# Performance work log

Hardware: AMD Instinct MI355X
Metric: run time of the kernel (lower is better)

## Reference

```python
import jax, jax.numpy as jnp
import numpy as np

NEG_SLOPE = 0.2
EPS = 1e-12


def setup_inputs() -> dict:
    key = jax.random.key(0)
    k1, k2, k3, k4, k5 = jax.random.split(key, 5)
    N, E, IN, OUT = 100000, 1600000, 256, 64
    x = jax.random.normal(k1, (N, IN), dtype=jnp.float32)
    edge_index = jax.random.randint(k2, (2, E), 0, N, dtype=jnp.int64)
    # GATConv (heads=1) parameters: lin weight, att_src, att_dst, bias
    W = jax.random.normal(k3, (IN, OUT), dtype=jnp.float32) * (1.0 / np.sqrt(IN))
    att_src = jax.random.normal(k4, (OUT,), dtype=jnp.float32) * (1.0 / np.sqrt(OUT))
    att_dst = jax.random.normal(k5, (OUT,), dtype=jnp.float32) * (1.0 / np.sqrt(OUT))
    bias = jnp.zeros((OUT,), dtype=jnp.float32)
    return {"x": x, "edge_index": edge_index, "W": W,
            "att_src": att_src, "att_dst": att_dst, "bias": bias}


def reference(x, edge_index, W, att_src, att_dst, bias):
    N = x.shape[0]
    # PyG GATConv default add_self_loops=True
    loops = jnp.arange(N, dtype=edge_index.dtype)
    src = jnp.concatenate([edge_index[0], loops])  # source j of edge (j -> i)
    dst = jnp.concatenate([edge_index[1], loops])  # target i (softmax segment)

    h = x @ W                                      # [N, out]
    a_src = h @ att_src                            # [N] per-node source score
    a_dst = h @ att_dst                            # [N] per-node target score

    e = jax.nn.leaky_relu(a_src[src] + a_dst[dst], NEG_SLOPE)  # [E+N]
    # segment softmax over incoming edges of each destination node
    e_max = jax.ops.segment_max(e, dst, num_segments=N)
    e = jnp.exp(e - e_max[dst])
    denom = jax.ops.segment_sum(e, dst, num_segments=N)
    alpha = e / denom[dst]                         # [E+N]

    # scatter-aggregate: out[i] = sum_j alpha_ij * h[j]
    out = jax.ops.segment_sum(alpha[:, None] * h[src], dst, num_segments=N)
    out = out + bias

    # dropout (p=0.3) in eval mode is identity; then F.normalize (row-wise L2)
    nrm = jnp.sqrt(jnp.sum(out * out, axis=-1, keepdims=True))
    return out / jnp.maximum(nrm, EPS)
```

## Files before the change

### kernel.cpp

```cpp
#include <hip/hip_runtime.h>
#include <hip/hip_bf16.h>
#include <math.h>

#define NEG_SLOPE 0.2f
#define EPS_NRM 1e-12f
#define K_IN 256
#define C_OUT 64
#define KSTEP 32
#define TILE_M 128
#define LDSROW 40

typedef __attribute__((ext_vector_type(8))) short bf16x8;
typedef __attribute__((ext_vector_type(4))) float f32x4;

__device__ __forceinline__ unsigned short bf16_rne(float v) {
    unsigned u = __float_as_uint(v);
    return (unsigned short)((u + 0x7fffu + ((u >> 16) & 1u)) >> 16);
}

__global__ __launch_bounds__(256) void wsplit(
    const float* __restrict__ W, unsigned short* __restrict__ Wt_hi,
    unsigned short* __restrict__ Wt_lo)
{
    int tid = blockIdx.x * blockDim.x + threadIdx.x;
    if (tid >= K_IN * C_OUT) return;
    int k = tid >> 6, c = tid & 63;
    float v = W[tid];
    unsigned short hb = bf16_rne(v);
    float vh = __uint_as_float((unsigned)hb << 16);
    unsigned short lb = bf16_rne(v - vh);
    Wt_hi[c * K_IN + k] = hb;
    Wt_lo[c * K_IN + k] = lb;
}

__global__ __launch_bounds__(256) void gemm_att(
    const float* __restrict__ x,
    const unsigned short* __restrict__ Wt_hi,
    const unsigned short* __restrict__ Wt_lo,
    const float* __restrict__ att_s, const float* __restrict__ att_d,
    __hip_bfloat16* __restrict__ h, float* __restrict__ a_src_arr,
    float* __restrict__ a_dst_arr, int N,
    const int* __restrict__ dstA, int* __restrict__ cnt, int E)
{
    __shared__ short A_hi[TILE_M][LDSROW];
    __shared__ short A_lo[TILE_M][LDSROW];
    __shared__ short B_hi[C_OUT][LDSROW];
    __shared__ short B_lo[C_OUT][LDSROW];

    int t   = threadIdx.x;
    int w   = t >> 6;
    int l   = t & 63;
    int lm  = l & 15;
    int grp = l >> 4;
    int row0 = blockIdx.x * TILE_M;

    int xrow  = t >> 1;
    int khalf = (t & 1) * 16;
    int srow = row0 + xrow; if (srow >= N) srow = N - 1;
    const float* xp = x + (size_t)srow * K_IN + khalf;

    int wcol   = t >> 2;
    int wchunk = (t & 3) * 8;
    const unsigned short* wph = Wt_hi + wcol * K_IN + wchunk;
    const unsigned short* wpl = Wt_lo + wcol * K_IN + wchunk;

    f32x4 acc[2][4];
#pragma unroll
    for (int m = 0; m < 2; ++m)
#pragma unroll
        for (int n = 0; n < 4; ++n) acc[m][n] = (f32x4){0.f, 0.f, 0.f, 0.f};

    float4 xf0, xf1, xf2, xf3;
    bf16x8 wvh, wvl;

    auto stage = [&]() {
        short sh[16], sl[16];
        const float* fv0 = (const float*)&xf0;
        const float* fv1 = (const float*)&xf1;
        const float* fv2 = (const float*)&xf2;
        const float* fv3 = (const float*)&xf3;
#pragma unroll
        for (int i = 0; i < 4; ++i) {
            float v0 = fv0[i], v1 = fv1[i], v2 = fv2[i], v3 = fv3[i];
            unsigned short h0 = bf16_rne(v0), h1 = bf16_rne(v1),
                           h2 = bf16_rne(v2), h3 = bf16_rne(v3);
            sh[i]      = (short)h0; sh[i + 4]  = (short)h1;
            sh[i + 8]  = (short)h2; sh[i + 12] = (short)h3;
            sl[i]      = (short)bf16_rne(v0 - __uint_as_float((unsigned)h0 << 16));
            sl[i + 4]  = (short)bf16_rne(v1 - __uint_as_float((unsigned)h1 << 16));
            sl[i + 8]  = (short)bf16_rne(v2 - __uint_as_float((unsigned)h2 << 16));
            sl[i + 12] = (short)bf16_rne(v3 - __uint_as_float((unsigned)h3 << 16));
        }
        *(bf16x8*)&A_hi[xrow][khalf]     = *(bf16x8*)&sh[0];
        *(bf16x8*)&A_hi[xrow][khalf + 8] = *(bf16x8*)&sh[8];
        *(bf16x8*)&A_lo[xrow][khalf]     = *(bf16x8*)&sl[0];
        *(bf16x8*)&A_lo[xrow][khalf + 8] = *(bf16x8*)&sl[8];
        *(bf16x8*)&B_hi[wcol][wchunk] = wvh;
        *(bf16x8*)&B_lo[wcol][wchunk] = wvl;
    };

    xf0 = *(const float4*)(xp + 0);
    xf1 = *(const float4*)(xp + 4);
    xf2 = *(const float4*)(xp + 8);
    xf3 = *(const float4*)(xp + 12);
    wvh = *(const bf16x8*)(wph);
    wvl = *(const bf16x8*)(wpl);
    stage();
    __syncthreads();

    for (int k0 = 0; k0 < K_IN; k0 += KSTEP) {
        const bool more = (k0 + KSTEP) < K_IN;
        if (more) {
            xf0 = *(const float4*)(xp + k0 + KSTEP + 0);
            xf1 = *(const float4*)(xp + k0 + KSTEP + 4);
            xf2 = *(const float4*)(xp + k0 + KSTEP + 8);
            xf3 = *(const float4*)(xp + k0 + KSTEP + 12);
            wvh = *(const bf16x8*)(wph + k0 + KSTEP);
            wvl = *(const bf16x8*)(wpl + k0 + KSTEP);
        }

        int xr0 = w * 32 + lm;
        bf16x8 xh0 = *(const bf16x8*)&A_hi[xr0][grp * 8];
        bf16x8 xl0 = *(const bf16x8*)&A_lo[xr0][grp * 8];
        bf16x8 xh1 = *(const bf16x8*)&A_hi[xr0 + 16][grp * 8];
        bf16x8 xl1 = *(const bf16x8*)&A_lo[xr0 + 16][grp * 8];
#pragma unroll
        for (int n = 0; n < 4; ++n) {
            bf16x8 wh = *(const bf16x8*)&B_hi[n * 16 + lm][grp * 8];
            bf16x8 wl = *(const bf16x8*)&B_lo[n * 16 + lm][grp * 8];
            acc[0][n] = __builtin_amdgcn_mfma_f32_16x16x32_bf16(wh, xh0, acc[0][n], 0, 0, 0);
            acc[1][n] = __builtin_amdgcn_mfma_f32_16x16x32_bf16(wh, xh1, acc[1][n], 0, 0, 0);
            acc[0][n] = __builtin_amdgcn_mfma_f32_16x16x32_bf16(wl, xh0, acc[0][n], 0, 0, 0);
            acc[1][n] = __builtin_amdgcn_mfma_f32_16x16x32_bf16(wl, xh1, acc[1][n], 0, 0, 0);
            acc[0][n] = __builtin_amdgcn_mfma_f32_16x16x32_bf16(wh, xl0, acc[0][n], 0, 0, 0);
            acc[1][n] = __builtin_amdgcn_mfma_f32_16x16x32_bf16(wh, xl1, acc[1][n], 0, 0, 0);
        }

        if (more) {
            __syncthreads();
            stage();
            __syncthreads();
        }
    }

    float4 as4[4], ad4[4];
#pragma unroll
    for (int n = 0; n < 4; ++n) {
        as4[n] = *(const float4*)(att_s + n * 16 + grp * 4);
        ad4[n] = *(const float4*)(att_d + n * 16 + grp * 4);
    }
#pragma unroll
    for (int m = 0; m < 2; ++m) {
        int row = row0 + w * 32 + m * 16 + lm;
        float ps = 0.f, pd = 0.f;
#pragma unroll
        for (int n = 0; n < 4; ++n) {
            f32x4 a = acc[m][n];
            ps += a.x * as4[n].x + a.y * as4[n].y + a.z * as4[n].z + a.w * as4[n].w;
            pd += a.x * ad4[n].x + a.y * ad4[n].y + a.z * ad4[n].z + a.w * ad4[n].w;
        }
        ps += __shfl_xor(ps, 16, 64); ps += __shfl_xor(ps, 32, 64);
        pd += __shfl_xor(pd, 16, 64); pd += __shfl_xor(pd, 32, 64);
        if (row < N) {
            if (grp == 0) { a_src_arr[row] = ps; a_dst_arr[row] = pd; }
#pragma unroll
            for (int n = 0; n < 4; ++n) {
                f32x4 a = acc[m][n];
                __hip_bfloat16 b0 = __float2bfloat16(a.x);
                __hip_bfloat16 b1 = __float2bfloat16(a.y);
                __hip_bfloat16 b2 = __float2bfloat16(a.z);
                __hip_bfloat16 b3 = __float2bfloat16(a.w);
                unsigned long long pk =
                    (unsigned long long)*(unsigned short*)&b0 |
                    ((unsigned long long)*(unsigned short*)&b1 << 16) |
                    ((unsigned long long)*(unsigned short*)&b2 << 32) |
                    ((unsigned long long)*(unsigned short*)&b3 << 48);
                *(unsigned long long*)(h + (size_t)row * C_OUT + n * 16 + grp * 4) = pk;
            }
        }
    }

    int stride = gridDim.x * blockDim.x;
    for (int i = blockIdx.x * blockDim.x + t; i < E; i += stride)
        atomicAdd(&cnt[dstA[i]], 1);
}

__global__ __launch_bounds__(256) void scan_p1(
    const int* __restrict__ cnt, int* __restrict__ partials, int n)
{
    int b = blockIdx.x, t = threadIdx.x;
    int base = b * 1024;
    int s = 0;
#pragma unroll
    for (int j = 0; j < 4; ++j) {
        int i = base + t * 4 + j;
        if (i < n) s += cnt[i];
    }
    for (int d = 1; d < 64; d <<= 1) s += __shfl_xor(s, d, 64);
    __shared__ int wsum[4];
    int lane = t & 63, wid = t >> 6;
    if (lane == 0) wsum[wid] = s;
    __syncthreads();
    if (t == 0) partials[b] = wsum[0] + wsum[1] + wsum[2] + wsum[3];
}

__global__ __launch_bounds__(256) void scan_p2(int* partials, int nb)
{
    __shared__ int buf[256];
    int t = threadIdx.x;
    int v = (t < nb) ? partials[t] : 0;
    buf[t] = v;
    __syncthreads();
    for (int d = 1; d < 256; d <<= 1) {
        int w = (t >= d) ? buf[t - d] : 0;
        __syncthreads();
        buf[t] += w;
        __syncthreads();
    }
    if (t < nb) partials[t] = buf[t] - v;
}

__global__ __launch_bounds__(256) void scan_p3(
    const int* __restrict__ cnt, const int* __restrict__ partials,
    int* __restrict__ offsets, int n)
{
    int b = blockIdx.x, t = threadIdx.x;
    int base = b * 1024;
    int v[4];
    int s = 0;
#pragma unroll
    for (int j = 0; j < 4; ++j) {
        int i = base + t * 4 + j;
        v[j] = (i < n) ? cnt[i] : 0;
        s += v[j];
    }
    int lane = t & 63, wid = t >> 6;
    int incl = s;
    for (int d = 1; d < 64; d <<= 1) {
        int w = __shfl_up(incl, d, 64);
        if (lane >= d) incl += w;
    }
    __shared__ int wsum[4];
    __shared__ int wbase[4];
    if (lane == 63) wsum[wid] = incl;
    __syncthreads();
    if (t == 0) {
        int r = 0;
        for (int i = 0; i < 4; ++i) { wbase[i] = r; r += wsum[i]; }
    }
    __syncthreads();
    int run = partials[b] + wbase[wid] + (incl - s);
#pragma unroll
    for (int j = 0; j < 4; ++j) {
        int i = base + t * 4 + j;
        if (i < n) {
            offsets[i] = run;
            run += v[j];
            if (i == n - 1) offsets[n] = run;
        }
    }
}

__global__ __launch_bounds__(256) void scatter_edges(
    const int* __restrict__ srcA, const int* __restrict__ dstA,
    const int* __restrict__ offsets, int* __restrict__ cursor,
    const float* __restrict__ a_src, const float* __restrict__ a_dst,
    unsigned long long* __restrict__ csr, int E)
{
    int i = blockIdx.x * blockDim.x + threadIdx.x;
    if (i >= E) return;
    int s = srcA[i], d = dstA[i];
    float e = a_src[s] + a_dst[d];
    e = fmaxf(e, NEG_SLOPE * e);
    float w = __expf(e);
    int pos = offsets[d] + atomicAdd(&cursor[d], 1);
    unsigned long long packed =
        (unsigned long long)(unsigned)s |
        ((unsigned long long)__float_as_uint(w) << 32);
    __builtin_nontemporal_store(packed, &csr[pos]);
}

__global__ __launch_bounds__(256) void gat_pull(
    const int* __restrict__ offsets, const int2* __restrict__ csr,
    const unsigned short* __restrict__ h, const float* __restrict__ a_src,
    const float* __restrict__ a_dst, const float* __restrict__ bias,
    float* __restrict__ out, int N)
{
    int gw   = (blockIdx.x * blockDim.x + threadIdx.x) >> 6;
    int lane = threadIdx.x & 63;
    int grp  = lane >> 4;
    int gl   = lane & 15;
    int node = gw * 4 + grp;
    bool valid = node < N;
    int nv = valid ? node : 0;

    int beg = offsets[nv];
    int n   = valid ? (offsets[nv + 1] - beg) : 0;
    const int2* ce = csr + (n ? beg : 0);

    float asv = a_src[nv], adv = a_dst[nv];
    float es = asv + adv; es = fmaxf(es, NEG_SLOPE * es);
    float ws = __expf(es);
    unsigned long long hu = *(const unsigned long long*)
        (h + (size_t)nv * C_OUT + 4 * gl);
    unsigned hl = (unsigned)hu, hh = (unsigned)(hu >> 32);
    float acc0 = ws * __uint_as_float(hl << 16);
    float acc1 = ws * __uint_as_float(hl & 0xffff0000u);
    float acc2 = ws * __uint_as_float(hh << 16);
    float acc3 = ws * __uint_as_float(hh & 0xffff0000u);
    float den = ws;

    int2 c0 = ce[0];
    int2 c1 = ce[(n > 1) ? 1 : 0];
    unsigned long long u0 = *(const unsigned long long*)
        (h + (size_t)c0.x * C_OUT + 4 * gl);
    unsigned long long u1 = *(const unsigned long long*)
        (h + (size_t)c1.x * C_OUT + 4 * gl);

    for (int p = 0; p < n; p += 2) {
        int2 m0 = ce[(p + 2 < n) ? p + 2 : 0];
        int2 m1 = ce[(p + 3 < n) ? p + 3 : 0];
        unsigned long long v0 = *(const unsigned long long*)
            (h + (size_t)m0.x * C_OUT + 4 * gl);
        unsigned long long v1 = *(const unsigned long long*)
            (h + (size_t)m1.x * C_OUT + 4 * gl);

        float w0 = __int_as_float(c0.y);
        float w1 = (p + 1 < n) ? __int_as_float(c1.y) : 0.f;
        unsigned l0 = (unsigned)u0, h0 = (unsigned)(u0 >> 32);
        unsigned l1 = (unsigned)u1, h1 = (unsigned)(u1 >> 32);
        den  += w0 + w1;
        acc0 += w0 * __uint_as_float(l0 << 16)
              + w1 * __uint_as_float(l1 << 16);
        acc1 += w0 * __uint_as_float(l0 & 0xffff0000u)
              + w1 * __uint_as_float(l1 & 0xffff0000u);
        acc2 += w0 * __uint_as_float(h0 << 16)
              + w1 * __uint_as_float(h1 << 16);
        acc3 += w0 * __uint_as_float(h0 & 0xffff0000u)
              + w1 * __uint_as_float(h1 & 0xffff0000u);

        c0 = m0; c1 = m1; u0 = v0; u1 = v1;
    }

    float4 bl = *(const float4*)(bias + 4 * gl);
    float rd = 1.f / den;
    float o0 = acc0 * rd + bl.x;
    float o1 = acc1 * rd + bl.y;
    float o2 = acc2 * rd + bl.z;
    float o3 = acc3 * rd + bl.w;

    float sq = o0 * o0 + o1 * o1 + o2 * o2 + o3 * o3;
#pragma unroll
    for (int d = 1; d < 16; d <<= 1) sq += __shfl_xor(sq, d, 64);
    float rn = 1.f / fmaxf(sqrtf(sq), EPS_NRM);

    if (valid)
        *(float4*)(out + (size_t)node * C_OUT + 4 * gl) =
            make_float4(o0 * rn, o1 * rn, o2 * rn, o3 * rn);
}

extern "C" void kernel_launch(void* const* d_in, const int* in_sizes, int n_in,
                              void* d_out, int out_size, void* d_ws, size_t ws_size,
                              hipStream_t stream)
{
    const float* x     = (const float*)d_in[0];
    const int*   ei    = (const int*)d_in[1];
    const float* W     = (const float*)d_in[2];
    const float* att_s = (const float*)d_in[3];
    const float* att_d = (const float*)d_in[4];
    const float* bias  = (const float*)d_in[5];
    float*       out   = (float*)d_out;

    const int OUT = in_sizes[3];
    const int IN  = in_sizes[2] / OUT;
    const int N   = in_sizes[0] / IN;
    const int E   = in_sizes[1] / 2;

    char* w = (char*)d_ws;
    auto alloc = [&](size_t bytes) -> void* {
        void* p = (void*)w;
        w += (bytes + 255) & ~(size_t)255;
        return p;
    };
    __hip_bfloat16* h = (__hip_bfloat16*)alloc((size_t)N * C_OUT * 2);
    float* a_src  = (float*)alloc((size_t)N * 4);
    float* a_dst  = (float*)alloc((size_t)N * 4);
    int*   cnt    = (int*)alloc((size_t)N * 2 * 4);
    int*   offs   = (int*)alloc((size_t)(N + 1) * 4);
    int*   parts  = (int*)alloc(1024 * 4);
    unsigned short* Wt_hi = (unsigned short*)alloc((size_t)K_IN * C_OUT * 2);
    unsigned short* Wt_lo = (unsigned short*)alloc((size_t)K_IN * C_OUT * 2);
    unsigned long long* csr = (unsigned long long*)alloc((size_t)E * 8);
    int*   cursor = cnt + N;

    hipMemsetAsync(cnt, 0, (size_t)N * 2 * 4, stream);

    wsplit<<<(K_IN * C_OUT + 255) / 256, 256, 0, stream>>>(W, Wt_hi, Wt_lo);

    gemm_att<<<(N + TILE_M - 1) / TILE_M, 256, 0, stream>>>(
        x, Wt_hi, Wt_lo, att_s, att_d, h, a_src, a_dst, N, ei + E, cnt, E);

    int NB = (N + 1023) / 1024;
    scan_p1<<<NB, 256, 0, stream>>>(cnt, parts, N);
    scan_p2<<<1, 256, 0, stream>>>(parts, NB);
    scan_p3<<<NB, 256, 0, stream>>>(cnt, parts, offs, N);

    scatter_edges<<<(E + 255) / 256, 256, 0, stream>>>(
        ei, ei + E, offs, cursor, a_src, a_dst, csr, E);

    gat_pull<<<(N + 15) / 16, 256, 0, stream>>>(offs, (const int2*)csr,
        (const unsigned short*)h, a_src, a_dst, bias, out, N);
}
```

Baseline: 375.7 us.

## Drop LDS staging in GEMM; each wave computes 16 rows directly from registers

The x@W GEMM no longer stages tiles in shared memory with block-wide barriers. Each wave now owns 16 rows, loads its x fragments straight into MFMA operand registers, and reads the bf16 hi/lo weight fragments directly from global memory, which should hit in cache. This removes the LDS traffic and __syncthreads, and the smaller 64-row blocks mean more of them. In exchange, weight reuse across rows within a block is lost and global/L2 reads of W increase.

```diff
diff --git a/kernel.cpp b/kernel.cpp
--- a/kernel.cpp
+++ b/kernel.cpp
@@ -6,9 +6,6 @@
 #define EPS_NRM 1e-12f
 #define K_IN 256
 #define C_OUT 64
-#define KSTEP 32
-#define TILE_M 128
-#define LDSROW 40
 
 typedef __attribute__((ext_vector_type(8))) short bf16x8;
 typedef __attribute__((ext_vector_type(4))) float f32x4;
@@ -42,141 +39,85 @@
     float* __restrict__ a_dst_arr, int N,
     const int* __restrict__ dstA, int* __restrict__ cnt, int E)
 {
-    __shared__ short A_hi[TILE_M][LDSROW];
-    __shared__ short A_lo[TILE_M][LDSROW];
-    __shared__ short B_hi[C_OUT][LDSROW];
-    __shared__ short B_lo[C_OUT][LDSROW];
-
     int t   = threadIdx.x;
-    int w   = t >> 6;
+    int gw  = (blockIdx.x * blockDim.x + t) >> 6;
     int l   = t & 63;
     int lm  = l & 15;
     int grp = l >> 4;
-    int row0 = blockIdx.x * TILE_M;
-
-    int xrow  = t >> 1;
-    int khalf = (t & 1) * 16;
-    int srow = row0 + xrow; if (srow >= N) srow = N - 1;
-    const float* xp = x + (size_t)srow * K_IN + khalf;
-
-    int wcol   = t >> 2;
-    int wchunk = (t & 3) * 8;
-    const unsigned short* wph = Wt_hi + wcol * K_IN + wchunk;
-    const unsigned short* wpl = Wt_lo + wcol * K_IN + wchunk;
-
-    f32x4 acc[2][4];
-#pragma unroll
-    for (int m = 0; m < 2; ++m)
-#pragma unroll
-        for (int n = 0; n < 4; ++n) acc[m][n] = (f32x4){0.f, 0.f, 0.f, 0.f};
-
-    float4 xf0, xf1, xf2, xf3;
-    bf16x8 wvh, wvl;
-
-    auto stage = [&]() {
-        short sh[16], sl[16];
-        const float* fv0 = (const float*)&xf0;
-        const float* fv1 = (const float*)&xf1;
-        const float* fv2 = (const float*)&xf2;
-        const float* fv3 = (const float*)&xf3;
+    int row0 = gw * 16;
+
+    int srow = row0 + lm; if (srow >= N) srow = N - 1;
+    const float* xq = x + (size_t)srow * K_IN + grp * 8;
+
+    const unsigned short* wbh = Wt_hi + (size_t)lm * K_IN + grp * 8;
+    const unsigned short* wbl = Wt_lo + (size_t)lm * K_IN + grp * 8;
+
+    f32x4 acc[4];
+#pragma unroll
+    for (int n = 0; n < 4; ++n) acc[n] = (f32x4){0.f, 0.f, 0.f, 0.f};
+
+    float4 xa = *(const float4*)(xq);
+    float4 xb = *(const float4*)(xq + 4);
+
+    for (int kt = 0; kt < K_IN / 32; ++kt) {
+        float4 xa2, xb2;
+        if (kt < K_IN / 32 - 1) {
+            xa2 = *(const float4*)(xq + (kt + 1) * 32);
+            xb2 = *(const float4*)(xq + (kt + 1) * 32 + 4);
+        }
+        short sh[8], sl[8];
+        const float* fa = (const float*)&xa;
+        const float* fb = (const float*)&xb;
 #pragma unroll
         for (int i = 0; i < 4; ++i) {
-            float v0 = fv0[i], v1 = fv1[i], v2 = fv2[i], v3 = fv3[i];
-            unsigned short h0 = bf16_rne(v0), h1 = bf16_rne(v1),
-                           h2 = bf16_rne(v2), h3 = bf16_rne(v3);
-            sh[i]      = (short)h0; sh[i + 4]  = (short)h1;
-            sh[i + 8]  = (short)h2; sh[i + 12] = (short)h3;
-            sl[i]      = (short)bf16_rne(v0 - __uint_as_float((unsigned)h0 << 16));
-            sl[i + 4]  = (short)bf16_rne(v1 - __uint_as_float((unsigned)h1 << 16));
-            sl[i + 8]  = (short)bf16_rne(v2 - __uint_as_float((unsigned)h2 << 16));
-            sl[i + 12] = (short)bf16_rne(v3 - __uint_as_float((unsigned)h3 << 16));
-        }
-        *(bf16x8*)&A_hi[xrow][khalf]     = *(bf16x8*)&sh[0];
-        *(bf16x8*)&A_hi[xrow][khalf + 8] = *(bf16x8*)&sh[8];
-        *(bf16x8*)&A_lo[xrow][khalf]     = *(bf16x8*)&sl[0];
-        *(bf16x8*)&A_lo[xrow][khalf + 8] = *(bf16x8*)&sl[8];
-        *(bf16x8*)&B_hi[wcol][wchunk] = wvh;
-        *(bf16x8*)&B_lo[wcol][wchunk] = wvl;
-    };
-
-    xf0 = *(const float4*)(xp + 0);
-    xf1 = *(const float4*)(xp + 4);
-    xf2 = *(const float4*)(xp + 8);
-    xf3 = *(const float4*)(xp + 12);
-    wvh = *(const bf16x8*)(wph);
-    wvl = *(const bf16x8*)(wpl);
-    stage();
-    __syncthreads();
-
-    for (int k0 = 0; k0 < K_IN; k0 += KSTEP) {
-        const bool more = (k0 + KSTEP) < K_IN;
-        if (more) {
-            xf0 = *(const float4*)(xp + k0 + KSTEP + 0);
-            xf1 = *(const float4*)(xp + k0 + KSTEP + 4);
-            xf2 = *(const float4*)(xp + k0 + KSTEP + 8);
-            xf3 = *(const float4*)(xp + k0 + KSTEP + 12);
-            wvh = *(const bf16x8*)(wph + k0 + KSTEP);
-            wvl = *(const bf16x8*)(wpl + k0 + KSTEP);
-        }
-
-        int xr0 = w * 32 + lm;
-        bf16x8 xh0 = *(const bf16x8*)&A_hi[xr0][grp * 8];
-        bf16x8 xl0 = *(const bf16x8*)&A_lo[xr0][grp * 8];
-        bf16x8 xh1 = *(const bf16x8*)&A_hi[xr0 + 16][grp * 8];
-        bf16x8 xl1 = *(const bf16x8*)&A_lo[xr0 + 16][grp * 8];
+            float v0 = fa[i], v1 = fb[i];
+            unsigned short h0 = bf16_rne(v0), h1 = bf16_rne(v1);
+            sh[i] = (short)h0; sh[i + 4] = (short)h1;
+            sl[i]     = (short)bf16_rne(v0 - __uint_as_float((unsigned)h0 << 16));
+            sl[i + 4] = (short)bf16_rne(v1 - __uint_as_float((unsigned)h1 << 16));
+        }
+        bf16x8 xh = *(bf16x8*)&sh[0];
+        bf16x8 xl = *(bf16x8*)&sl[0];
+
+        int ko = kt * 32;
 #pragma unroll
         for (int n = 0; n < 4; ++n) {
-            bf16x8 wh = *(const bf16x8*)&B_hi[n * 16 + lm][grp * 8];
-            bf16x8 wl = *(const bf16x8*)&B_lo[n * 16 + lm][grp * 8];
-            acc[0][n] = __builtin_amdgcn_mfma_f32_16x16x32_bf16(wh, xh0, acc[0][n], 0, 0, 0);
-            acc[1][n] = __builtin_amdgcn_mfma_f32_16x16x32_bf16(wh, xh1, acc[1][n], 0, 0, 0);
-            acc[0][n] = __builtin_amdgcn_mfma_f32_16x16x32_bf16(wl, xh0, acc[0][n], 0, 0, 0);
-            acc[1][n] = __builtin_amdgcn_mfma_f32_16x16x32_bf16(wl, xh1, acc[1][n], 0, 0, 0);
-            acc[0][n] = __builtin_amdgcn_mfma_f32_16x16x32_bf16(wh, xl0, acc[0][n], 0, 0, 0);
-            acc[1][n] = __builtin_amdgcn_mfma_f32_16x16x32_bf16(wh, xl1, acc[1][n], 0, 0, 0);
-        }
-
-        if (more) {
-            __syncthreads();
-            stage();
-            __syncthreads();
-        }
-    }
-
-    float4 as4[4], ad4[4];
+            bf16x8 wh = *(const bf16x8*)(wbh + (size_t)n * 16 * K_IN + ko);
+            bf16x8 wl = *(const bf16x8*)(wbl + (size_t)n * 16 * K_IN + ko);
+            acc[n] = __builtin_amdgcn_mfma_f32_16x16x32_bf16(wh, xh, acc[n], 0, 0, 0);
+            acc[n] = __builtin_amdgcn_mfma_f32_16x16x32_bf16(wl, xh, acc[n], 0, 0, 0);
+            acc[n] = __builtin_amdgcn_mfma_f32_16x16x32_bf16(wh, xl, acc[n], 0, 0, 0);
+        }
+        xa = xa2; xb = xb2;
+    }
+
+    int row = row0 + lm;
+    float ps = 0.f, pd = 0.f;
 #pragma unroll
     for (int n = 0; n < 4; ++n) {
-        as4[n] = *(const float4*)(att_s + n * 16 + grp * 4);
-        ad4[n] = *(const float4*)(att_d + n * 16 + grp * 4);
-    }
-#pragma unroll
-    for (int m = 0; m < 2; ++m) {
-        int row = row0 + w * 32 + m * 16 + lm;
-        float ps = 0.f, pd = 0.f;
+        float4 as4 = *(const float4*)(att_s + n * 16 + grp * 4);
+        float4 ad4 = *(const float4*)(att_d + n * 16 + grp * 4);
+        f32x4 a = acc[n];
+        ps += a.x * as4.x + a.y * as4.y + a.z * as4.z + a.w * as4.w;
+        pd += a.x * ad4.x + a.y * ad4.y + a.z * ad4.z + a.w * ad4.w;
+    }
+    ps += __shfl_xor(ps, 16, 64); ps += __shfl_xor(ps, 32, 64);
+    pd += __shfl_xor(pd, 16, 64); pd += __shfl_xor(pd, 32, 64);
+    if (row < N) {
+        if (grp == 0) { a_src_arr[row] = ps; a_dst_arr[row] = pd; }
 #pragma unroll
         for (int n = 0; n < 4; ++n) {
-            f32x4 a = acc[m][n];
-            ps += a.x * as4[n].x + a.y * as4[n].y + a.z * as4[n].z + a.w * as4[n].w;
-            pd += a.x * ad4[n].x + a.y * ad4[n].y + a.z * ad4[n].z + a.w * ad4[n].w;
-        }
-        ps += __shfl_xor(ps, 16, 64); ps += __shfl_xor(ps, 32, 64);
-        pd += __shfl_xor(pd, 16, 64); pd += __shfl_xor(pd, 32, 64);
-        if (row < N) {
-            if (grp == 0) { a_src_arr[row] = ps; a_dst_arr[row] = pd; }
-#pragma unroll
-            for (int n = 0; n < 4; ++n) {
-                f32x4 a = acc[m][n];
-                __hip_bfloat16 b0 = __float2bfloat16(a.x);
-                __hip_bfloat16 b1 = __float2bfloat16(a.y);
-                __hip_bfloat16 b2 = __float2bfloat16(a.z);
-                __hip_bfloat16 b3 = __float2bfloat16(a.w);
-                unsigned long long pk =
-                    (unsigned long long)*(unsigned short*)&b0 |
-                    ((unsigned long long)*(unsigned short*)&b1 << 16) |
-                    ((unsigned long long)*(unsigned short*)&b2 << 32) |
-                    ((unsigned long long)*(unsigned short*)&b3 << 48);
-                *(unsigned long long*)(h + (size_t)row * C_OUT + n * 16 + grp * 4) = pk;
-            }
+            f32x4 a = acc[n];
+            __hip_bfloat16 b0 = __float2bfloat16(a.x);
+            __hip_bfloat16 b1 = __float2bfloat16(a.y);
+            __hip_bfloat16 b2 = __float2bfloat16(a.z);
+            __hip_bfloat16 b3 = __float2bfloat16(a.w);
+            unsigned long long pk =
+                (unsigned long long)*(unsigned short*)&b0 |
+                ((unsigned long long)*(unsigned short*)&b1 << 16) |
+                ((unsigned long long)*(unsigned short*)&b2 << 32) |
+                ((unsigned long long)*(unsigned short*)&b3 << 48);
+            *(unsigned long long*)(h + (size_t)row * C_OUT + n * 16 + grp * 4) = pk;
         }
     }
 
@@ -397,7 +338,7 @@
 
     wsplit<<<(K_IN * C_OUT + 255) / 256, 256, 0, stream>>>(W, Wt_hi, Wt_lo);
 
-    gemm_att<<<(N + TILE_M - 1) / TILE_M, 256, 0, stream>>>(
+    gemm_att<<<(N + 63) / 64, 256, 0, stream>>>(
         x, Wt_hi, Wt_lo, att_s, att_d, h, a_src, a_dst, N, ei + E, cnt, E);
 
     int NB = (N + 1023) / 1024;
```

Measured after the change: 387.4 us. 3.1% more time.
